# Kernel tuning notes

Hardware: AMD Instinct MI355X
Metric: run time of the kernel (lower is better)

## Reference

```python
import jax, jax.numpy as jnp
import numpy as np

N_ENT, N_REL, N_TIME, N_METAREL = 20000, 400, 366, 800
E, PE = 200000, 80000
ENT, REL, TIME = 160, 160, 80
NUM_LAYERS = 2
NL = 2 * NUM_LAYERS + 2  # enc layers + dec layers + mean + log_std
DIN_E = REL + ENT + TIME
DIN_R = 2 * REL


def setup_inputs() -> dict:
    key = jax.random.key(0)
    ks = jax.random.split(key, 40)
    s = 0.05
    inp = {
        "ent_feat": jax.random.normal(ks[0], (N_ENT, ENT), jnp.float32),
        "rel_feat": jax.random.normal(ks[1], (N_REL, REL), jnp.float32),
        "time_emb": jax.random.normal(ks[2], (N_TIME, TIME), jnp.float32),
        "metarel_emb": jax.random.normal(ks[3], (N_METAREL, REL), jnp.float32),
        "noise_e": jax.random.normal(ks[4], (N_ENT, ENT), jnp.float32),
        "noise_r": jax.random.normal(ks[5], (N_REL, REL), jnp.float32),
        "ent_WI_w": jax.random.normal(ks[6], (NL, DIN_E, ENT), jnp.float32) * s,
        "ent_WI_b": jnp.zeros((NL, ENT), jnp.float32),
        "ent_WO_w": jax.random.normal(ks[7], (NL, DIN_E, ENT), jnp.float32) * s,
        "ent_WO_b": jnp.zeros((NL, ENT), jnp.float32),
        "ent_WS_w": jax.random.normal(ks[8], (NL, ENT, ENT), jnp.float32) * s,
        "ent_WS_b": jnp.zeros((NL, ENT), jnp.float32),
        "ent_WT_w": jax.random.normal(ks[9], (NL, TIME, TIME), jnp.float32) * s,
        "ent_WT_b": jnp.zeros((NL, TIME), jnp.float32),
        "rel_WI_w": jax.random.normal(ks[10], (NL, DIN_R, REL), jnp.float32) * s,
        "rel_WI_b": jnp.zeros((NL, REL), jnp.float32),
        "rel_WO_w": jax.random.normal(ks[11], (NL, DIN_R, REL), jnp.float32) * s,
        "rel_WO_b": jnp.zeros((NL, REL), jnp.float32),
        "rel_WS_w": jax.random.normal(ks[12], (NL, REL, REL), jnp.float32) * s,
        "rel_WS_b": jnp.zeros((NL, REL), jnp.float32),
        "rel_WM_w": jax.random.normal(ks[13], (NL, REL, REL), jnp.float32) * s,
        "rel_WM_b": jnp.zeros((NL, REL), jnp.float32),
        "src": jax.random.randint(ks[14], (E,), 0, N_ENT, jnp.int32),
        "dst": jax.random.randint(ks[15], (E,), 0, N_ENT, jnp.int32),
        "e_rel": jax.random.randint(ks[16], (E,), 0, N_REL, jnp.int32),
        "e_time": jax.random.randint(ks[17], (E,), 0, N_TIME, jnp.int32),
        "e_inv": jax.random.randint(ks[18], (E,), 0, 2, jnp.int32),
        "p_src": jax.random.randint(ks[19], (PE,), 0, N_REL, jnp.int32),
        "p_dst": jax.random.randint(ks[20], (PE,), 0, N_REL, jnp.int32),
        "p_rel": jax.random.randint(ks[21], (PE,), 0, N_METAREL, jnp.int32),
        "p_inv": jax.random.randint(ks[22], (PE,), 0, 2, jnp.int32),
    }
    return inp


def _mean_agg(msg, dst, n_nodes):
    # DGL fn.mean: zero for nodes with no in-edges
    s = jax.ops.segment_sum(msg, dst, num_segments=n_nodes)
    c = jax.ops.segment_sum(jnp.ones((msg.shape[0], 1), msg.dtype), dst, num_segments=n_nodes)
    return jnp.where(c > 0, s / jnp.maximum(c, 1.0), jnp.zeros_like(s))


def _ent_layer(p, i, ent, rel, tim, src, dst, e_rel, e_time, e_inv, act):
    (WIw, WIb, WOw, WOb, WSw, WSb, WTw, WTb) = p
    comp = jnp.concatenate([rel[e_rel], ent[src], tim[e_time]], axis=-1)  # [E, rel+ent+time]
    msg = jnp.where((e_inv == 0)[:, None], comp @ WIw[i] + WIb[i], comp @ WOw[i] + WOb[i])
    h_agg = _mean_agg(msg, dst, ent.shape[0])
    h = ent @ WSw[i] + WSb[i] + h_agg
    t = tim @ WTw[i] + WTb[i]
    if act:
        h, t = jax.nn.relu(h), jax.nn.relu(t)
    return h, t


def _rel_layer(p, i, rel, meta, p_src, p_dst, p_rel, p_inv, act):
    (WIw, WIb, WOw, WOb, WSw, WSb, WMw, WMb) = p
    comp = jnp.concatenate([meta[p_rel], rel[p_src]], axis=-1)  # [PE, 2*rel]
    msg = jnp.where((p_inv == 0)[:, None], comp @ WIw[i] + WIb[i], comp @ WOw[i] + WOb[i])
    h_agg = _mean_agg(msg, p_dst, rel.shape[0])
    h = rel @ WSw[i] + WSb[i] + h_agg
    m = meta @ WMw[i] + WMb[i]
    if act:
        h, m = jax.nn.relu(h), jax.nn.relu(m)
    return h, m


def _vgae(ent, rel, tim, meta, noise_e, noise_r, pe, pr, g, pg):
    L = NUM_LAYERS
    # encoder GNN: layers 0..L-1
    for i in range(L):
        act = i < L - 1
        ent, tim = _ent_layer(pe, i, ent, rel, tim, *g, act)
        rel, meta = _rel_layer(pr, i, rel, meta, *pg, act)
    # variational heads: indices 2L (mean), 2L+1 (log_std), act=None
    mean_e = _ent_layer(pe, 2 * L, ent, rel, tim, *g, False)[0]
    log_std_e = _ent_layer(pe, 2 * L + 1, ent, rel, tim, *g, False)[0]
    mean_r = _rel_layer(pr, 2 * L, rel, meta, *pg, False)[0]
    log_std_r = _rel_layer(pr, 2 * L + 1, rel, meta, *pg, False)[0]
    z_e = mean_e + noise_e * jnp.exp(log_std_e)
    z_r = mean_r + noise_r * jnp.exp(log_std_r)
    # decoder GNN: layers L..2L-1, starting from sampled z
    ent_o, rel_o, tim_o, meta_o = z_e, z_r, tim, meta
    for i in range(L):
        act = i < L - 1
        ent_o, tim_o = _ent_layer(pe, L + i, ent_o, rel_o, tim_o, *g, act)
        rel_o, meta_o = _rel_layer(pr, L + i, rel_o, meta_o, *pg, act)
    return (ent, ent_o, rel, rel_o, tim, tim_o, meta, meta_o)


def reference(ent_feat, rel_feat, time_emb, metarel_emb, noise_e, noise_r,
              ent_WI_w, ent_WI_b, ent_WO_w, ent_WO_b, ent_WS_w, ent_WS_b, ent_WT_w, ent_WT_b,
              rel_WI_w, rel_WI_b, rel_WO_w, rel_WO_b, rel_WS_w, rel_WS_b, rel_WM_w, rel_WM_b,
              src, dst, e_rel, e_time, e_inv, p_src, p_dst, p_rel, p_inv):
    pe = (ent_WI_w, ent_WI_b, ent_WO_w, ent_WO_b, ent_WS_w, ent_WS_b, ent_WT_w, ent_WT_b)
    pr = (rel_WI_w, rel_WI_b, rel_WO_w, rel_WO_b, rel_WS_w, rel_WS_b, rel_WM_w, rel_WM_b)
    g = (src, dst, e_rel, e_time, e_inv)
    pg = (p_src, p_dst, p_rel, p_inv)
    return _vgae(ent_feat, rel_feat, time_emb, metarel_emb, noise_e, noise_r, pe, pr, g, pg)
```

## Files before the change

kernel.cpp:

```cpp
#include <hip/hip_runtime.h>
#include <math.h>

#define N_ENT     20000
#define N_RELN    400
#define N_TIME    366
#define N_META    800
#define NE        200000
#define NPE       80000

typedef __attribute__((ext_vector_type(8))) short short8;
typedef __attribute__((ext_vector_type(4))) float f32x4;

static __device__ __forceinline__ ushort f2bf(float x) {
    unsigned u = __float_as_uint(x);
    unsigned r = (u + 0x7FFF + ((u >> 16) & 1)) >> 16;
    return (ushort)r;
}
static __device__ __forceinline__ float bf2f(ushort b) {
    return __uint_as_float(((unsigned)b) << 16);
}

struct BPrep { const float* W[18]; };

__global__ __launch_bounds__(256) void bprep(BPrep bp, ushort* __restrict__ hi, ushort* __restrict__ lo)
{
    int idx = blockIdx.x * 256 + threadIdx.x;
    if (idx >= 18 * 160 * 20) return;
    int s = idx / 3200, rem = idx - s * 3200;
    int n = rem / 20, kc = rem - n * 20;
    const float* __restrict__ W = bp.W[s];
    ushort h[8], l[8];
#pragma unroll
    for (int j = 0; j < 8; ++j) {
        float x = W[(kc * 8 + j) * 160 + n];
        h[j] = f2bf(x);
        l[j] = f2bf(x - bf2f(h[j]));
    }
    size_t o = (size_t)s * 25600 + n * 160 + kc * 8;
    *(short8*)(hi + o) = *(short8*)h;
    *(short8*)(lo + o) = *(short8*)l;
}

__global__ __launch_bounds__(256) void aprep(const float* __restrict__ in,
                                             ushort* __restrict__ hi, ushort* __restrict__ lo, int n8)
{
    int i = blockIdx.x * 256 + threadIdx.x;
    if (i >= n8) return;
    const float* p = in + (size_t)i * 8;
    ushort h[8], l[8];
#pragma unroll
    for (int j = 0; j < 8; ++j) {
        float x = p[j];
        h[j] = f2bf(x);
        l[j] = f2bf(x - bf2f(h[j]));
    }
    *(short8*)(hi + (size_t)i * 8) = *(short8*)h;
    *(short8*)(lo + (size_t)i * 8) = *(short8*)l;
}

struct BigMF {
    const ushort* bh[3];
    const ushort* bl[3];
    const float*  bias[3];
    float*        C[3];
};

__global__ __launch_bounds__(256, 4) void gemm_big_mfma(
    const ushort* __restrict__ Ah, const ushort* __restrict__ Al, int M, BigMF bb)
{
    __shared__ ushort Ahi[64][40], Alo[64][40];
    __shared__ ushort Bhi[160][40], Blo[160][40];
    const int z = blockIdx.z;
    const ushort* __restrict__ Bh = bb.bh[z];
    const ushort* __restrict__ Bl = bb.bl[z];
    const float*  __restrict__ bias = bb.bias[z];
    float* __restrict__ C = bb.C[z];
    const int m0 = blockIdx.x * 64;
    const int t  = threadIdx.x;
    const int lane = t & 63, w = t >> 6;
    const int fr = lane & 15, fq = lane >> 4;

    f32x4 acc[10];
#pragma unroll
    for (int i = 0; i < 10; ++i) acc[i] = (f32x4){0.f, 0.f, 0.f, 0.f};

    for (int k0 = 0; k0 < 160; k0 += 32) {
        {
            int r = t >> 2, kc = t & 3;
            int row = m0 + r;
            short8 vh = {0,0,0,0,0,0,0,0}, vl = {0,0,0,0,0,0,0,0};
            if (row < M) {
                size_t o = (size_t)row * 160 + k0 + kc * 8;
                vh = *(const short8*)(Ah + o);
                vl = *(const short8*)(Al + o);
            }
            *(short8*)&Ahi[r][kc * 8] = vh;
            *(short8*)&Alo[r][kc * 8] = vl;
        }
#pragma unroll
        for (int i = 0; i < 3; ++i) {
            int idx = t + i * 256;
            if (idx < 640) {
                int col = idx >> 2, kc = idx & 3;
                size_t o = (size_t)col * 160 + k0 + kc * 8;
                *(short8*)&Bhi[col][kc * 8] = *(const short8*)(Bh + o);
                *(short8*)&Blo[col][kc * 8] = *(const short8*)(Bl + o);
            }
        }
        __syncthreads();
        short8 ah = *(const short8*)&Ahi[w * 16 + fr][fq * 8];
        short8 al = *(const short8*)&Alo[w * 16 + fr][fq * 8];
#pragma unroll
        for (int tt = 0; tt < 10; ++tt) {
            short8 bh = *(const short8*)&Bhi[tt * 16 + fr][fq * 8];
            short8 bl = *(const short8*)&Blo[tt * 16 + fr][fq * 8];
            acc[tt] = __builtin_amdgcn_mfma_f32_16x16x32_bf16(ah, bh, acc[tt], 0, 0, 0);
            acc[tt] = __builtin_amdgcn_mfma_f32_16x16x32_bf16(al, bh, acc[tt], 0, 0, 0);
            acc[tt] = __builtin_amdgcn_mfma_f32_16x16x32_bf16(ah, bl, acc[tt], 0, 0, 0);
        }
        __syncthreads();
    }
#pragma unroll
    for (int tt = 0; tt < 10; ++tt) {
        int col = tt * 16 + fr;
        float bv = bias ? bias[col] : 0.f;
#pragma unroll
        for (int q = 0; q < 4; ++q) {
            int row = m0 + w * 16 + fq * 4 + q;
            if (row < M) C[(size_t)row * 160 + col] = acc[tt][q] + bv;
        }
    }
}

struct SmallDesc {
    const float* A;
    const float* B;
    const float* bias;
    float*       C;
    int M, K, N, ldb, relu;
};
struct SmallBatch { SmallDesc d[18]; };

#define FMA4(acc, a, b) { acc.x = fmaf(a, b.x, acc.x); acc.y = fmaf(a, b.y, acc.y); \
                          acc.z = fmaf(a, b.z, acc.z); acc.w = fmaf(a, b.w, acc.w); }

__global__ __launch_bounds__(256) void gemm_small_batch(SmallBatch sb)
{
    SmallDesc dd = sb.d[blockIdx.y];
    int tid = blockIdx.x * 256 + threadIdx.x;
    int ng = dd.N >> 2;
    int mb = tid / ng;
    int nmb = (dd.M + 3) >> 2;
    if (mb >= nmb) return;
    int g = tid - mb * ng;
    int r0 = mb * 4;
    int mlast = dd.M - 1;
    const float* A0 = dd.A + (size_t)min(r0 + 0, mlast) * dd.K;
    const float* A1 = dd.A + (size_t)min(r0 + 1, mlast) * dd.K;
    const float* A2 = dd.A + (size_t)min(r0 + 2, mlast) * dd.K;
    const float* A3 = dd.A + (size_t)min(r0 + 3, mlast) * dd.K;
    const float* Bp = dd.B + g * 4;
    float4 c0 = {0,0,0,0}, c1 = {0,0,0,0}, c2 = {0,0,0,0}, c3 = {0,0,0,0};
    for (int k = 0; k < dd.K; k += 4) {
        float4 b0 = *(const float4*)(Bp + (size_t)(k + 0) * dd.ldb);
        float4 b1 = *(const float4*)(Bp + (size_t)(k + 1) * dd.ldb);
        float4 b2 = *(const float4*)(Bp + (size_t)(k + 2) * dd.ldb);
        float4 b3 = *(const float4*)(Bp + (size_t)(k + 3) * dd.ldb);
        float4 a0 = *(const float4*)(A0 + k);
        float4 a1 = *(const float4*)(A1 + k);
        float4 a2 = *(const float4*)(A2 + k);
        float4 a3 = *(const float4*)(A3 + k);
        FMA4(c0, a0.x, b0) FMA4(c0, a0.y, b1) FMA4(c0, a0.z, b2) FMA4(c0, a0.w, b3)
        FMA4(c1, a1.x, b0) FMA4(c1, a1.y, b1) FMA4(c1, a1.z, b2) FMA4(c1, a1.w, b3)
        FMA4(c2, a2.x, b0) FMA4(c2, a2.y, b1) FMA4(c2, a2.z, b2) FMA4(c2, a2.w, b3)
        FMA4(c3, a3.x, b0) FMA4(c3, a3.y, b1) FMA4(c3, a3.z, b2) FMA4(c3, a3.w, b3)
    }
    float4 bv = {0,0,0,0};
    if (dd.bias) bv = *(const float4*)(dd.bias + g * 4);
    c0.x += bv.x; c0.y += bv.y; c0.z += bv.z; c0.w += bv.w;
    c1.x += bv.x; c1.y += bv.y; c1.z += bv.z; c1.w += bv.w;
    c2.x += bv.x; c2.y += bv.y; c2.z += bv.z; c2.w += bv.w;
    c3.x += bv.x; c3.y += bv.y; c3.z += bv.z; c3.w += bv.w;
    if (dd.relu) {
        c0.x = fmaxf(c0.x, 0.f); c0.y = fmaxf(c0.y, 0.f); c0.z = fmaxf(c0.z, 0.f); c0.w = fmaxf(c0.w, 0.f);
        c1.x = fmaxf(c1.x, 0.f); c1.y = fmaxf(c1.y, 0.f); c1.z = fmaxf(c1.z, 0.f); c1.w = fmaxf(c1.w, 0.f);
        c2.x = fmaxf(c2.x, 0.f); c2.y = fmaxf(c2.y, 0.f); c2.z = fmaxf(c2.z, 0.f); c2.w = fmaxf(c2.w, 0.f);
        c3.x = fmaxf(c3.x, 0.f); c3.y = fmaxf(c3.y, 0.f); c3.z = fmaxf(c3.z, 0.f); c3.w = fmaxf(c3.w, 0.f);
    }
    float* C = dd.C + (size_t)r0 * dd.N + g * 4;
    if (r0 + 0 < dd.M) *(float4*)(C + 0 * (size_t)dd.N) = c0;
    if (r0 + 1 < dd.M) *(float4*)(C + 1 * (size_t)dd.N) = c1;
    if (r0 + 2 < dd.M) *(float4*)(C + 2 * (size_t)dd.N) = c2;
    if (r0 + 3 < dd.M) *(float4*)(C + 3 * (size_t)dd.N) = c3;
}

__global__ void count_deg(const int* __restrict__ d, int E, int* __restrict__ cnt)
{
    int e = blockIdx.x * 256 + threadIdx.x;
    if (e < E) atomicAdd(&cnt[d[e]], 1);
}

__global__ __launch_bounds__(256) void scan_excl(int* __restrict__ cnt, int* __restrict__ rowptr, int n)
{
    __shared__ int ssum[256];
    int t = threadIdx.x;
    int chunk = (n + 255) / 256;
    int s0 = t * chunk; if (s0 > n) s0 = n;
    int s1 = s0 + chunk; if (s1 > n) s1 = n;
    int local = 0;
    for (int i = s0; i < s1; ++i) local += cnt[i];
    ssum[t] = local;
    __syncthreads();
    if (t == 0) {
        int acc = 0;
        for (int i = 0; i < 256; ++i) { int v = ssum[i]; ssum[i] = acc; acc += v; }
        rowptr[n] = acc;
    }
    __syncthreads();
    int acc = ssum[t];
    for (int i = s0; i < s1; ++i) {
        int v = cnt[i];
        rowptr[i] = acc;
        cnt[i] = acc;
        acc += v;
    }
}

__global__ void scatter_pack(const int* __restrict__ d, const int* __restrict__ a0,
                             const int* __restrict__ a1, const int* __restrict__ a2,
                             const int* __restrict__ inv, int E,
                             int* __restrict__ cursor, int4* __restrict__ pack)
{
    int e = blockIdx.x * 256 + threadIdx.x;
    if (e < E) {
        int p = atomicAdd(&cursor[d[e]], 1);
        int4 v;
        v.x = a0[e]; v.y = a1[e]; v.z = a2 ? a2[e] : 0; v.w = inv[e];
        pack[p] = v;
    }
}

__global__ __launch_bounds__(256) void agg_ent_csr(
    const int* __restrict__ rowptr, const int4* __restrict__ pack,
    const float* __restrict__ arI, const float* __restrict__ arO,
    const float* __restrict__ aeI, const float* __restrict__ aeO,
    const float* __restrict__ atI, const float* __restrict__ atO,
    float* __restrict__ H, int relu)
{
    int tid = blockIdx.x * 256 + threadIdx.x;
    int n = tid / 40;
    if (n >= N_ENT) return;
    int g = tid - n * 40;
    int c = g * 4;
    int b = rowptr[n], e = rowptr[n + 1];
    float ax = 0.f, ay = 0.f, az = 0.f, aw = 0.f;
    for (int j = b; j < e; ++j) {
        int4 p = pack[j];
        const float* t1 = (p.w ? arO : arI) + (size_t)p.x * 160 + c;
        const float* t2 = (p.w ? aeO : aeI) + (size_t)p.y * 160 + c;
        const float* t3 = (p.w ? atO : atI) + (size_t)p.z * 160 + c;
        float4 v1 = *(const float4*)t1;
        float4 v2 = *(const float4*)t2;
        float4 v3 = *(const float4*)t3;
        ax += v1.x + v2.x + v3.x;
        ay += v1.y + v2.y + v3.y;
        az += v1.z + v2.z + v3.z;
        aw += v1.w + v2.w + v3.w;
    }
    size_t idx = (size_t)n * 160 + c;
    float4 h = *(const float4*)(H + idx);
    if (e > b) {
        float s = 1.0f / (float)(e - b);
        h.x = fmaf(ax, s, h.x); h.y = fmaf(ay, s, h.y);
        h.z = fmaf(az, s, h.z); h.w = fmaf(aw, s, h.w);
    }
    if (relu) {
        h.x = fmaxf(h.x, 0.f); h.y = fmaxf(h.y, 0.f);
        h.z = fmaxf(h.z, 0.f); h.w = fmaxf(h.w, 0.f);
    }
    *(float4*)(H + idx) = h;
}

__global__ __launch_bounds__(256) void agg_ent_sample(
    const int* __restrict__ rowptr, const int4* __restrict__ pack,
    const float* __restrict__ arI, const float* __restrict__ arO,
    const float* __restrict__ aeI, const float* __restrict__ aeO,
    const float* __restrict__ atI, const float* __restrict__ atO,
    const float* __restrict__ Hs, const float* __restrict__ mean,
    const float* __restrict__ noise, float* __restrict__ out)
{
    int tid = blockIdx.x * 256 + threadIdx.x;
    int n = tid / 40;
    if (n >= N_ENT) return;
    int g = tid - n * 40;
    int c = g * 4;
    int b = rowptr[n], e = rowptr[n + 1];
    float ax = 0.f, ay = 0.f, az = 0.f, aw = 0.f;
    for (int j = b; j < e; ++j) {
        int4 p = pack[j];
        const float* t1 = (p.w ? arO : arI) + (size_t)p.x * 160 + c;
        const float* t2 = (p.w ? aeO : aeI) + (size_t)p.y * 160 + c;
        const float* t3 = (p.w ? atO : atI) + (size_t)p.z * 160 + c;
        float4 v1 = *(const float4*)t1;
        float4 v2 = *(const float4*)t2;
        float4 v3 = *(const float4*)t3;
        ax += v1.x + v2.x + v3.x;
        ay += v1.y + v2.y + v3.y;
        az += v1.z + v2.z + v3.z;
        aw += v1.w + v2.w + v3.w;
    }
    size_t idx = (size_t)n * 160 + c;
    float4 h = *(const float4*)(Hs + idx);
    if (e > b) {
        float s = 1.0f / (float)(e - b);
        h.x = fmaf(ax, s, h.x); h.y = fmaf(ay, s, h.y);
        h.z = fmaf(az, s, h.z); h.w = fmaf(aw, s, h.w);
    }
    float4 mn = *(const float4*)(mean + idx);
    float4 nz = *(const float4*)(noise + idx);
    float4 zv;
    zv.x = fmaf(nz.x, expf(h.x), mn.x);
    zv.y = fmaf(nz.y, expf(h.y), mn.y);
    zv.z = fmaf(nz.z, expf(h.z), mn.z);
    zv.w = fmaf(nz.w, expf(h.w), mn.w);
    *(float4*)(out + idx) = zv;
}

__global__ __launch_bounds__(512) void agg_rel_fused(
    const int* __restrict__ rowptr, const int4* __restrict__ pack,
    const float* __restrict__ bmI, const float* __restrict__ bmO,
    const float* __restrict__ brI, const float* __restrict__ brO,
    float* __restrict__ H, int relu)
{
    __shared__ float part[12][40][4];
    int n = blockIdx.x;
    int t = threadIdx.x;
    int g = t % 40, s = t / 40;
    int b = rowptr[n], e = rowptr[n + 1];
    if (s < 12) {
        int c = g * 4;
        float ax = 0.f, ay = 0.f, az = 0.f, aw = 0.f;
        for (int j = b + s; j < e; j += 12) {
            int4 p = pack[j];
            const float* pm = (p.w ? bmO : bmI) + (size_t)p.x * 160 + c;
            const float* pr = (p.w ? brO : brI) + (size_t)p.y * 160 + c;
            float4 vm = *(const float4*)pm;
            float4 vr = *(const float4*)pr;
            ax += vm.x + vr.x; ay += vm.y + vr.y;
            az += vm.z + vr.z; aw += vm.w + vr.w;
        }
        part[s][g][0] = ax; part[s][g][1] = ay;
        part[s][g][2] = az; part[s][g][3] = aw;
    }
    __syncthreads();
    if (t < 160) {
        int gg = t >> 2, q = t & 3;
        float acc = 0.f;
#pragma unroll
        for (int s2 = 0; s2 < 12; ++s2) acc += part[s2][gg][q];
        size_t idx = (size_t)n * 160 + t;
        float h = H[idx];
        int d = e - b;
        if (d > 0) h = fmaf(acc, 1.0f / (float)d, h);
        if (relu) h = fmaxf(h, 0.f);
        H[idx] = h;
    }
}

__global__ __launch_bounds__(512) void agg_rel_sample(
    const int* __restrict__ rowptr, const int4* __restrict__ pack,
    const float* __restrict__ bmI, const float* __restrict__ bmO,
    const float* __restrict__ brI, const float* __restrict__ brO,
    const float* __restrict__ Hs, const float* __restrict__ mean,
    const float* __restrict__ noise, float* __restrict__ out)
{
    __shared__ float part[12][40][4];
    int n = blockIdx.x;
    int t = threadIdx.x;
    int g = t % 40, s = t / 40;
    int b = rowptr[n], e = rowptr[n + 1];
    if (s < 12) {
        int c = g * 4;
        float ax = 0.f, ay = 0.f, az = 0.f, aw = 0.f;
        for (int j = b + s; j < e; j += 12) {
            int4 p = pack[j];
            const float* pm = (p.w ? bmO : bmI) + (size_t)p.x * 160 + c;
            const float* pr = (p.w ? brO : brI) + (size_t)p.y * 160 + c;
            float4 vm = *(const float4*)pm;
            float4 vr = *(const float4*)pr;
            ax += vm.x + vr.x; ay += vm.y + vr.y;
            az += vm.z + vr.z; aw += vm.w + vr.w;
        }
        part[s][g][0] = ax; part[s][g][1] = ay;
        part[s][g][2] = az; part[s][g][3] = aw;
    }
    __syncthreads();
    if (t < 160) {
        int gg = t >> 2, q = t & 3;
        float acc = 0.f;
#pragma unroll
        for (int s2 = 0; s2 < 12; ++s2) acc += part[s2][gg][q];
        size_t idx = (size_t)n * 160 + t;
        float h = Hs[idx];
        int d = e - b;
        if (d > 0) h = fmaf(acc, 1.0f / (float)d, h);
        out[idx] = fmaf(noise[idx], expf(h), mean[idx]);
    }
}

extern "C" void kernel_launch(void* const* d_in, const int* in_sizes, int n_in,
                              void* d_out, int out_size, void* d_ws, size_t ws_size,
                              hipStream_t stream)
{
    const float* ent0   = (const float*)d_in[0];
    const float* rel0   = (const float*)d_in[1];
    const float* tim0   = (const float*)d_in[2];
    const float* meta0  = (const float*)d_in[3];
    const float* noiseE = (const float*)d_in[4];
    const float* noiseR = (const float*)d_in[5];
    const float* entWI  = (const float*)d_in[6];
    const float* entWIb = (const float*)d_in[7];
    const float* entWO  = (const float*)d_in[8];
    const float* entWOb = (const float*)d_in[9];
    const float* entWS  = (const float*)d_in[10];
    const float* entWSb = (const float*)d_in[11];
    const float* entWT  = (const float*)d_in[12];
    const float* entWTb = (const float*)d_in[13];
    const float* relWI  = (const float*)d_in[14];
    const float* relWIb = (const float*)d_in[15];
    const float* relWO  = (const float*)d_in[16];
    const float* relWOb = (const float*)d_in[17];
    const float* relWS  = (const float*)d_in[18];
    const float* relWSb = (const float*)d_in[19];
    const float* relWM  = (const float*)d_in[20];
    const float* relWMb = (const float*)d_in[21];
    const int* src    = (const int*)d_in[22];
    const int* dst    = (const int*)d_in[23];
    const int* e_rel  = (const int*)d_in[24];
    const int* e_time = (const int*)d_in[25];
    const int* e_inv  = (const int*)d_in[26];
    const int* p_src  = (const int*)d_in[27];
    const int* p_dst  = (const int*)d_in[28];
    const int* p_rel  = (const int*)d_in[29];
    const int* p_inv  = (const int*)d_in[30];

    float* out = (float*)d_out;
    float* OUT_ent   = out + 0;
    float* OUT_ento  = out + 3200000;
    float* OUT_rel   = out + 6400000;
    float* OUT_relo  = out + 6464000;
    float* OUT_tim   = out + 6528000;
    float* OUT_timo  = out + 6557280;
    float* OUT_meta  = out + 6586560;
    float* OUT_metao = out + 6714560;

    char* wsp = (char*)d_ws;
    size_t off = 0;
    auto allocF = [&](size_t n) -> float* {
        float* p = (float*)(wsp + off);
        off += ((n * sizeof(float) + 255) & ~(size_t)255);
        return p;
    };
    auto allocU = [&](size_t n) -> ushort* {
        ushort* p = (ushort*)(wsp + off);
        off += ((n * sizeof(ushort) + 255) & ~(size_t)255);
        return p;
    };
    auto allocI = [&](size_t n) -> int* {
        int* p = (int*)(wsp + off);
        off += ((n * sizeof(int) + 255) & ~(size_t)255);
        return p;
    };
    float* AI      = allocF(3200000);
    float* AO      = allocF(3200000);
    float* B1v     = allocF(3200000);
    float* B5v     = allocF(3200000);
    float* tim1    = allocF(29280);
    float* tim_o1  = allocF(29280);
    float* rel1    = allocF(64000);
    float* rel_o1  = allocF(64000);
    float* meta1   = allocF(128000);
    float* meta_o1 = allocF(128000);
    float* arI  = allocF(64000);
    float* arO  = allocF(64000);
    float* atI  = allocF(58560);
    float* atO  = allocF(58560);
    float* bmI  = allocF(128000);
    float* bmO  = allocF(128000);
    float* brI  = allocF(64000);
    float* brO  = allocF(64000);
    float* ar5I = allocF(64000);
    float* ar5O = allocF(64000);
    float* at5I = allocF(58560);
    float* at5O = allocF(58560);
    float* bm5I = allocF(128000);
    float* bm5O = allocF(128000);
    float* br5I = allocF(64000);
    float* br5O = allocF(64000);
    float* hR4  = allocF(64000);
    float* hR5  = allocF(64000);
    float* zR   = allocF(64000);
    ushort* Ahg = allocU(3200000);
    ushort* Alg = allocU(3200000);
    ushort* Bhg = allocU(18 * 25600);
    ushort* Blg = allocU(18 * 25600);
    int*  cntE    = allocI(N_ENT);
    int*  rowptrE = allocI(N_ENT + 1);
    int4* packE   = (int4*)allocI(NE * 4);
    int*  cntR    = allocI(N_RELN);
    int*  rowptrR = allocI(N_RELN + 1);
    int4* packR   = (int4*)allocI(NPE * 4);
    if (ws_size < off) return;

    hipMemsetAsync(cntE, 0, N_ENT * sizeof(int), stream);
    hipMemsetAsync(cntR, 0, N_RELN * sizeof(int), stream);
    count_deg<<<(NE + 255) / 256, 256, 0, stream>>>(dst, NE, cntE);
    count_deg<<<(NPE + 255) / 256, 256, 0, stream>>>(p_dst, NPE, cntR);
    scan_excl<<<1, 256, 0, stream>>>(cntE, rowptrE, N_ENT);
    scan_excl<<<1, 256, 0, stream>>>(cntR, rowptrR, N_RELN);
    scatter_pack<<<(NE + 255) / 256, 256, 0, stream>>>(dst, e_rel, src, e_time, e_inv, NE, cntE, packE);
    scatter_pack<<<(NPE + 255) / 256, 256, 0, stream>>>(p_dst, p_rel, p_src, nullptr, p_inv, NPE, cntR, packR);

    BPrep bp;
    for (int li = 0; li < 6; ++li) {
        bp.W[li * 3 + 0] = entWI + (size_t)li * 64000 + 25600;
        bp.W[li * 3 + 1] = entWO + (size_t)li * 64000 + 25600;
        bp.W[li * 3 + 2] = entWS + (size_t)li * 25600;
    }
    bprep<<<(18 * 160 * 20 + 255) / 256, 256, 0, stream>>>(bp, Bhg, Blg);

    auto big3 = [&](int li, float* entOut) {
        BigMF bb;
        for (int j = 0; j < 3; ++j) {
            bb.bh[j] = Bhg + (size_t)(li * 3 + j) * 25600;
            bb.bl[j] = Blg + (size_t)(li * 3 + j) * 25600;
        }
        bb.bias[0] = nullptr; bb.bias[1] = nullptr; bb.bias[2] = entWSb + li * 160;
        bb.C[0] = AI; bb.C[1] = AO; bb.C[2] = entOut;
        gemm_big_mfma<<<dim3(313, 1, 3), 256, 0, stream>>>(Ahg, Alg, N_ENT, bb);
    };
    auto prepA = [&](const float* entIn) {
        aprep<<<(400000 + 255) / 256, 256, 0, stream>>>(entIn, Ahg, Alg, 400000);
    };

    auto stage = [&](int li, const float* entIn, const float* relIn, const float* timIn,
                     const float* metaIn, float* entOut, float* timOut,
                     float* relOut, float* metaOut, int act) {
        const float* WI  = entWI + (size_t)li * 64000;
        const float* WO  = entWO + (size_t)li * 64000;
        const float* rWI = relWI + (size_t)li * 51200;
        const float* rWO = relWO + (size_t)li * 51200;

        SmallBatch sb{};
        int ns = 0;
        sb.d[ns++] = SmallDesc{relIn,  WI,          entWIb + li * 160, arI,    N_RELN, 160, 160, 160, 0};
        sb.d[ns++] = SmallDesc{relIn,  WO,          entWOb + li * 160, arO,    N_RELN, 160, 160, 160, 0};
        sb.d[ns++] = SmallDesc{timIn,  WI + 51200,  nullptr,           atI,    N_TIME,  80, 160, 160, 0};
        sb.d[ns++] = SmallDesc{timIn,  WO + 51200,  nullptr,           atO,    N_TIME,  80, 160, 160, 0};
        if (timOut)
            sb.d[ns++] = SmallDesc{timIn, entWT + (size_t)li * 6400, entWTb + li * 80,
                                   timOut, N_TIME, 80, 80, 80, act};
        sb.d[ns++] = SmallDesc{metaIn, rWI,         relWIb + li * 160, bmI,    N_META, 160, 160, 160, 0};
        sb.d[ns++] = SmallDesc{metaIn, rWO,         relWOb + li * 160, bmO,    N_META, 160, 160, 160, 0};
        sb.d[ns++] = SmallDesc{relIn,  rWI + 25600, nullptr,           brI,    N_RELN, 160, 160, 160, 0};
        sb.d[ns++] = SmallDesc{relIn,  rWO + 25600, nullptr,           brO,    N_RELN, 160, 160, 160, 0};
        sb.d[ns++] = SmallDesc{relIn,  relWS + (size_t)li * 25600, relWSb + li * 160,
                               relOut, N_RELN, 160, 160, 160, 0};
        if (metaOut)
            sb.d[ns++] = SmallDesc{metaIn, relWM + (size_t)li * 25600, relWMb + li * 160,
                                   metaOut, N_META, 160, 160, 160, act};
        gemm_small_batch<<<dim3(32, ns), 256, 0, stream>>>(sb);

        prepA(entIn);
        big3(li, entOut);
        agg_ent_csr<<<(N_ENT * 40 + 255) / 256, 256, 0, stream>>>(
            rowptrE, packE, arI, arO, AI, AO, atI, atO, entOut, act);
        agg_rel_fused<<<N_RELN, 512, 0, stream>>>(
            rowptrR, packR, bmI, bmO, brI, brO, relOut, act);
    };

    stage(0, ent0, rel0, tim0, meta0, B1v, tim1, rel1, meta1, 1);
    stage(1, B1v, rel1, tim1, meta1, OUT_ent, OUT_tim, OUT_rel, OUT_meta, 0);

    {
        const float* WI4  = entWI + (size_t)4 * 64000;
        const float* WO4  = entWO + (size_t)4 * 64000;
        const float* WI5  = entWI + (size_t)5 * 64000;
        const float* WO5  = entWO + (size_t)5 * 64000;
        const float* rWI4 = relWI + (size_t)4 * 51200;
        const float* rWO4 = relWO + (size_t)4 * 51200;
        const float* rWI5 = relWI + (size_t)5 * 51200;
        const float* rWO5 = relWO + (size_t)5 * 51200;

        SmallBatch sb{};
        int ns = 0;
        sb.d[ns++] = SmallDesc{OUT_rel,  WI4,          entWIb + 4 * 160, arI,  N_RELN, 160, 160, 160, 0};
        sb.d[ns++] = SmallDesc{OUT_rel,  WO4,          entWOb + 4 * 160, arO,  N_RELN, 160, 160, 160, 0};
        sb.d[ns++] = SmallDesc{OUT_tim,  WI4 + 51200,  nullptr,          atI,  N_TIME,  80, 160, 160, 0};
        sb.d[ns++] = SmallDesc{OUT_tim,  WO4 + 51200,  nullptr,          atO,  N_TIME,  80, 160, 160, 0};
        sb.d[ns++] = SmallDesc{OUT_meta, rWI4,         relWIb + 4 * 160, bmI,  N_META, 160, 160, 160, 0};
        sb.d[ns++] = SmallDesc{OUT_meta, rWO4,         relWOb + 4 * 160, bmO,  N_META, 160, 160, 160, 0};
        sb.d[ns++] = SmallDesc{OUT_rel,  rWI4 + 25600, nullptr,          brI,  N_RELN, 160, 160, 160, 0};
        sb.d[ns++] = SmallDesc{OUT_rel,  rWO4 + 25600, nullptr,          brO,  N_RELN, 160, 160, 160, 0};
        sb.d[ns++] = SmallDesc{OUT_rel,  relWS + (size_t)4 * 25600, relWSb + 4 * 160,
                               hR4, N_RELN, 160, 160, 160, 0};
        sb.d[ns++] = SmallDesc{OUT_rel,  WI5,          entWIb + 5 * 160, ar5I, N_RELN, 160, 160, 160, 0};
        sb.d[ns++] = SmallDesc{OUT_rel,  WO5,          entWOb + 5 * 160, ar5O, N_RELN, 160, 160, 160, 0};
        sb.d[ns++] = SmallDesc{OUT_tim,  WI5 + 51200,  nullptr,          at5I, N_TIME,  80, 160, 160, 0};
        sb.d[ns++] = SmallDesc{OUT_tim,  WO5 + 51200,  nullptr,          at5O, N_TIME,  80, 160, 160, 0};
        sb.d[ns++] = SmallDesc{OUT_meta, rWI5,         relWIb + 5 * 160, bm5I, N_META, 160, 160, 160, 0};
        sb.d[ns++] = SmallDesc{OUT_meta, rWO5,         relWOb + 5 * 160, bm5O, N_META, 160, 160, 160, 0};
        sb.d[ns++] = SmallDesc{OUT_rel,  rWI5 + 25600, nullptr,          br5I, N_RELN, 160, 160, 160, 0};
        sb.d[ns++] = SmallDesc{OUT_rel,  rWO5 + 25600, nullptr,          br5O, N_RELN, 160, 160, 160, 0};
        sb.d[ns++] = SmallDesc{OUT_rel,  relWS + (size_t)5 * 25600, relWSb + 5 * 160,
                               hR5, N_RELN, 160, 160, 160, 0};
        gemm_small_batch<<<dim3(32, ns), 256, 0, stream>>>(sb);

        prepA(OUT_ent);
        big3(4, B5v);
        agg_ent_csr<<<(N_ENT * 40 + 255) / 256, 256, 0, stream>>>(
            rowptrE, packE, arI, arO, AI, AO, atI, atO, B5v, 0);
        big3(5, B1v);
        agg_ent_sample<<<(N_ENT * 40 + 255) / 256, 256, 0, stream>>>(
            rowptrE, packE, ar5I, ar5O, AI, AO, at5I, at5O, B1v, B5v, noiseE, B5v);
        agg_rel_fused<<<N_RELN, 512, 0, stream>>>(
            rowptrR, packR, bmI, bmO, brI, brO, hR4, 0);
        agg_rel_sample<<<N_RELN, 512, 0, stream>>>(
            rowptrR, packR, bm5I, bm5O, br5I, br5O, hR5, hR4, noiseR, zR);
    }

    stage(2, B5v, zR, OUT_tim, OUT_meta, B1v, tim_o1, rel_o1, meta_o1, 1);
    stage(3, B1v, rel_o1, tim_o1, meta_o1, OUT_ento, OUT_timo, OUT_relo, OUT_metao, 0);
}
```

Baseline: 857.9 us.

## Merge independent kernels into role-dispatched launches to cut launch count

Independent work is packed into shared launches selected by blockIdx.y. The small GEMM batch now runs alongside the A-matrix bf16 split, the relation aggregation shares a launch with the big MFMA GEMM, and the entity and relation sampling heads are combined into one kernel. Graph preprocessing is also merged: one degree count, one 1024-thread warp-shuffle scan and one scatter handle both graphs. This removes launches and serialization gaps and lets the small relation work overlap the large GEMM, but the relation aggregation now uses 6 partial sums instead of 12, giving it less per-node parallelism.

```diff
diff --git a/kernel.cpp b/kernel.cpp
--- a/kernel.cpp
+++ b/kernel.cpp
@@ -39,97 +39,6 @@
     size_t o = (size_t)s * 25600 + n * 160 + kc * 8;
     *(short8*)(hi + o) = *(short8*)h;
     *(short8*)(lo + o) = *(short8*)l;
-}
-
-__global__ __launch_bounds__(256) void aprep(const float* __restrict__ in,
-                                             ushort* __restrict__ hi, ushort* __restrict__ lo, int n8)
-{
-    int i = blockIdx.x * 256 + threadIdx.x;
-    if (i >= n8) return;
-    const float* p = in + (size_t)i * 8;
-    ushort h[8], l[8];
-#pragma unroll
-    for (int j = 0; j < 8; ++j) {
-        float x = p[j];
-        h[j] = f2bf(x);
-        l[j] = f2bf(x - bf2f(h[j]));
-    }
-    *(short8*)(hi + (size_t)i * 8) = *(short8*)h;
-    *(short8*)(lo + (size_t)i * 8) = *(short8*)l;
-}
-
-struct BigMF {
-    const ushort* bh[3];
-    const ushort* bl[3];
-    const float*  bias[3];
-    float*        C[3];
-};
-
-__global__ __launch_bounds__(256, 4) void gemm_big_mfma(
-    const ushort* __restrict__ Ah, const ushort* __restrict__ Al, int M, BigMF bb)
-{
-    __shared__ ushort Ahi[64][40], Alo[64][40];
-    __shared__ ushort Bhi[160][40], Blo[160][40];
-    const int z = blockIdx.z;
-    const ushort* __restrict__ Bh = bb.bh[z];
-    const ushort* __restrict__ Bl = bb.bl[z];
-    const float*  __restrict__ bias = bb.bias[z];
-    float* __restrict__ C = bb.C[z];
-    const int m0 = blockIdx.x * 64;
-    const int t  = threadIdx.x;
-    const int lane = t & 63, w = t >> 6;
-    const int fr = lane & 15, fq = lane >> 4;
-
-    f32x4 acc[10];
-#pragma unroll
-    for (int i = 0; i < 10; ++i) acc[i] = (f32x4){0.f, 0.f, 0.f, 0.f};
-
-    for (int k0 = 0; k0 < 160; k0 += 32) {
-        {
-            int r = t >> 2, kc = t & 3;
-            int row = m0 + r;
-            short8 vh = {0,0,0,0,0,0,0,0}, vl = {0,0,0,0,0,0,0,0};
-            if (row < M) {
-                size_t o = (size_t)row * 160 + k0 + kc * 8;
-                vh = *(const short8*)(Ah + o);
-                vl = *(const short8*)(Al + o);
-            }
-            *(short8*)&Ahi[r][kc * 8] = vh;
-            *(short8*)&Alo[r][kc * 8] = vl;
-        }
-#pragma unroll
-        for (int i = 0; i < 3; ++i) {
-            int idx = t + i * 256;
-            if (idx < 640) {
-                int col = idx >> 2, kc = idx & 3;
-                size_t o = (size_t)col * 160 + k0 + kc * 8;
-                *(short8*)&Bhi[col][kc * 8] = *(const short8*)(Bh + o);
-                *(short8*)&Blo[col][kc * 8] = *(const short8*)(Bl + o);
-            }
-        }
-        __syncthreads();
-        short8 ah = *(const short8*)&Ahi[w * 16 + fr][fq * 8];
-        short8 al = *(const short8*)&Alo[w * 16 + fr][fq * 8];
-#pragma unroll
-        for (int tt = 0; tt < 10; ++tt) {
-            short8 bh = *(const short8*)&Bhi[tt * 16 + fr][fq * 8];
-            short8 bl = *(const short8*)&Blo[tt * 16 + fr][fq * 8];
-            acc[tt] = __builtin_amdgcn_mfma_f32_16x16x32_bf16(ah, bh, acc[tt], 0, 0, 0);
-            acc[tt] = __builtin_amdgcn_mfma_f32_16x16x32_bf16(al, bh, acc[tt], 0, 0, 0);
-            acc[tt] = __builtin_amdgcn_mfma_f32_16x16x32_bf16(ah, bl, acc[tt], 0, 0, 0);
-        }
-        __syncthreads();
-    }
-#pragma unroll
-    for (int tt = 0; tt < 10; ++tt) {
-        int col = tt * 16 + fr;
-        float bv = bias ? bias[col] : 0.f;
-#pragma unroll
-        for (int q = 0; q < 4; ++q) {
-            int row = m0 + w * 16 + fq * 4 + q;
-            if (row < M) C[(size_t)row * 160 + col] = acc[tt][q] + bv;
-        }
-    }
 }
 
 struct SmallDesc {
@@ -144,10 +53,28 @@
 #define FMA4(acc, a, b) { acc.x = fmaf(a, b.x, acc.x); acc.y = fmaf(a, b.y, acc.y); \
                           acc.z = fmaf(a, b.z, acc.z); acc.w = fmaf(a, b.w, acc.w); }
 
-__global__ __launch_bounds__(256) void gemm_small_batch(SmallBatch sb)
-{
-    SmallDesc dd = sb.d[blockIdx.y];
+__global__ __launch_bounds__(256) void stage_p1(SmallBatch sb, int ns,
+    const float* __restrict__ ain, ushort* __restrict__ ah, ushort* __restrict__ al, int nitems)
+{
+    int role = blockIdx.y;
     int tid = blockIdx.x * 256 + threadIdx.x;
+    if (role == ns) {
+        int stride = gridDim.x * 256;
+        for (int i = tid; i < nitems; i += stride) {
+            const float* p = ain + (size_t)i * 8;
+            ushort h[8], l[8];
+#pragma unroll
+            for (int j = 0; j < 8; ++j) {
+                float x = p[j];
+                h[j] = f2bf(x);
+                l[j] = f2bf(x - bf2f(h[j]));
+            }
+            *(short8*)(ah + (size_t)i * 8) = *(short8*)h;
+            *(short8*)(al + (size_t)i * 8) = *(short8*)l;
+        }
+        return;
+    }
+    SmallDesc dd = sb.d[role];
     int ng = dd.N >> 2;
     int mb = tid / ng;
     int nmb = (dd.M + 3) >> 2;
@@ -194,49 +121,124 @@
     if (r0 + 3 < dd.M) *(float4*)(C + 3 * (size_t)dd.N) = c3;
 }
 
-__global__ void count_deg(const int* __restrict__ d, int E, int* __restrict__ cnt)
-{
-    int e = blockIdx.x * 256 + threadIdx.x;
-    if (e < E) atomicAdd(&cnt[d[e]], 1);
-}
-
-__global__ __launch_bounds__(256) void scan_excl(int* __restrict__ cnt, int* __restrict__ rowptr, int n)
-{
-    __shared__ int ssum[256];
-    int t = threadIdx.x;
-    int chunk = (n + 255) / 256;
-    int s0 = t * chunk; if (s0 > n) s0 = n;
-    int s1 = s0 + chunk; if (s1 > n) s1 = n;
-    int local = 0;
-    for (int i = s0; i < s1; ++i) local += cnt[i];
-    ssum[t] = local;
+struct BigMF {
+    const ushort* bh[3];
+    const ushort* bl[3];
+    const float*  bias[3];
+    float*        C[3];
+};
+struct AggRelA {
+    const int* rowptr;
+    const int4* pack;
+    const float *bmI, *bmO, *brI, *brO;
+    float* H;
+    int relu;
+};
+
+__global__ __launch_bounds__(256, 4) void stage_p2(
+    const ushort* __restrict__ Ah, const ushort* __restrict__ Al, int M,
+    BigMF bb, AggRelA ar)
+{
+    __shared__ ushort Ahi[64][40], Alo[64][40];
+    __shared__ ushort Bhi[160][40], Blo[160][40];
+    __shared__ float part[6][40][4];
+    const int role = blockIdx.y;
+    const int t = threadIdx.x;
+
+    if (role < 3) {
+        const int m0 = blockIdx.x * 64;
+        if (m0 >= M) return;
+        const ushort* __restrict__ Bh = bb.bh[role];
+        const ushort* __restrict__ Bl = bb.bl[role];
+        const float*  __restrict__ bias = bb.bias[role];
+        float* __restrict__ C = bb.C[role];
+        const int lane = t & 63, w = t >> 6;
+        const int fr = lane & 15, fq = lane >> 4;
+
+        f32x4 acc[10];
+#pragma unroll
+        for (int i = 0; i < 10; ++i) acc[i] = (f32x4){0.f, 0.f, 0.f, 0.f};
+
+        for (int k0 = 0; k0 < 160; k0 += 32) {
+            {
+                int r = t >> 2, kc = t & 3;
+                int row = m0 + r;
+                short8 vh = {0,0,0,0,0,0,0,0}, vl = {0,0,0,0,0,0,0,0};
+                if (row < M) {
+                    size_t o = (size_t)row * 160 + k0 + kc * 8;
+                    vh = *(const short8*)(Ah + o);
+                    vl = *(const short8*)(Al + o);
+                }
+                *(short8*)&Ahi[r][kc * 8] = vh;
+                *(short8*)&Alo[r][kc * 8] = vl;
+            }
+#pragma unroll
+            for (int i = 0; i < 3; ++i) {
+                int idx = t + i * 256;
+                if (idx < 640) {
+                    int col = idx >> 2, kc = idx & 3;
+                    size_t o = (size_t)col * 160 + k0 + kc * 8;
+                    *(short8*)&Bhi[col][kc * 8] = *(const short8*)(Bh + o);
+                    *(short8*)&Blo[col][kc * 8] = *(const short8*)(Bl + o);
+                }
+            }
+            __syncthreads();
+            short8 ahv = *(const short8*)&Ahi[w * 16 + fr][fq * 8];
+            short8 alv = *(const short8*)&Alo[w * 16 + fr][fq * 8];
+#pragma unroll
+            for (int tt = 0; tt < 10; ++tt) {
+                short8 bh = *(const short8*)&Bhi[tt * 16 + fr][fq * 8];
+                short8 bl = *(const short8*)&Blo[tt * 16 + fr][fq * 8];
+                acc[tt] = __builtin_amdgcn_mfma_f32_16x16x32_bf16(ahv, bh, acc[tt], 0, 0, 0);
+                acc[tt] = __builtin_amdgcn_mfma_f32_16x16x32_bf16(alv, bh, acc[tt], 0, 0, 0);
+                acc[tt] = __builtin_amdgcn_mfma_f32_16x16x32_bf16(ahv, bl, acc[tt], 0, 0, 0);
+            }
+            __syncthreads();
+        }
+#pragma unroll
+        for (int tt = 0; tt < 10; ++tt) {
+            int col = tt * 16 + fr;
+            float bv = bias ? bias[col] : 0.f;
+#pragma unroll
+            for (int q = 0; q < 4; ++q) {
+                int row = m0 + w * 16 + fq * 4 + q;
+                if (row < M) C[(size_t)row * 160 + col] = acc[tt][q] + bv;
+            }
+        }
+        return;
+    }
+
+    int n = blockIdx.x;
+    if (n >= N_RELN) return;
+    int g = t % 40, s = t / 40;
+    int b = ar.rowptr[n], e = ar.rowptr[n + 1];
+    if (s < 6) {
+        int c = g * 4;
+        float ax = 0.f, ay = 0.f, az = 0.f, aw = 0.f;
+        for (int j = b + s; j < e; j += 6) {
+            int4 p = ar.pack[j];
+            const float* pm = (p.w ? ar.bmO : ar.bmI) + (size_t)p.x * 160 + c;
+            const float* pr = (p.w ? ar.brO : ar.brI) + (size_t)p.y * 160 + c;
+            float4 vm = *(const float4*)pm;
+            float4 vr = *(const float4*)pr;
+            ax += vm.x + vr.x; ay += vm.y + vr.y;
+            az += vm.z + vr.z; aw += vm.w + vr.w;
+        }
+        part[s][g][0] = ax; part[s][g][1] = ay;
+        part[s][g][2] = az; part[s][g][3] = aw;
+    }
     __syncthreads();
-    if (t == 0) {
-        int acc = 0;
-        for (int i = 0; i < 256; ++i) { int v = ssum[i]; ssum[i] = acc; acc += v; }
-        rowptr[n] = acc;
-    }
-    __syncthreads();
-    int acc = ssum[t];
-    for (int i = s0; i < s1; ++i) {
-        int v = cnt[i];
-        rowptr[i] = acc;
-        cnt[i] = acc;
-        acc += v;
-    }
-}
-
-__global__ void scatter_pack(const int* __restrict__ d, const int* __restrict__ a0,
-                             const int* __restrict__ a1, const int* __restrict__ a2,
-                             const int* __restrict__ inv, int E,
-                             int* __restrict__ cursor, int4* __restrict__ pack)
-{
-    int e = blockIdx.x * 256 + threadIdx.x;
-    if (e < E) {
-        int p = atomicAdd(&cursor[d[e]], 1);
-        int4 v;
-        v.x = a0[e]; v.y = a1[e]; v.z = a2 ? a2[e] : 0; v.w = inv[e];
-        pack[p] = v;
+    if (t < 160) {
+        int gg = t >> 2, q = t & 3;
+        float acc = 0.f;
+#pragma unroll
+        for (int s2 = 0; s2 < 6; ++s2) acc += part[s2][gg][q];
+        size_t idx = (size_t)n * 160 + t;
+        float h = ar.H[idx];
+        int d = e - b;
+        if (d > 0) h = fmaf(acc, 1.0f / (float)d, h);
+        if (ar.relu) h = fmaxf(h, 0.f);
+        ar.H[idx] = h;
     }
 }
 
@@ -281,67 +283,68 @@
     *(float4*)(H + idx) = h;
 }
 
-__global__ __launch_bounds__(256) void agg_ent_sample(
-    const int* __restrict__ rowptr, const int4* __restrict__ pack,
+__global__ __launch_bounds__(256) void heads_p3b(
+    const int* __restrict__ rowptrE, const int4* __restrict__ packE,
     const float* __restrict__ arI, const float* __restrict__ arO,
     const float* __restrict__ aeI, const float* __restrict__ aeO,
     const float* __restrict__ atI, const float* __restrict__ atO,
-    const float* __restrict__ Hs, const float* __restrict__ mean,
-    const float* __restrict__ noise, float* __restrict__ out)
-{
-    int tid = blockIdx.x * 256 + threadIdx.x;
-    int n = tid / 40;
-    if (n >= N_ENT) return;
-    int g = tid - n * 40;
-    int c = g * 4;
-    int b = rowptr[n], e = rowptr[n + 1];
-    float ax = 0.f, ay = 0.f, az = 0.f, aw = 0.f;
-    for (int j = b; j < e; ++j) {
-        int4 p = pack[j];
-        const float* t1 = (p.w ? arO : arI) + (size_t)p.x * 160 + c;
-        const float* t2 = (p.w ? aeO : aeI) + (size_t)p.y * 160 + c;
-        const float* t3 = (p.w ? atO : atI) + (size_t)p.z * 160 + c;
-        float4 v1 = *(const float4*)t1;
-        float4 v2 = *(const float4*)t2;
-        float4 v3 = *(const float4*)t3;
-        ax += v1.x + v2.x + v3.x;
-        ay += v1.y + v2.y + v3.y;
-        az += v1.z + v2.z + v3.z;
-        aw += v1.w + v2.w + v3.w;
-    }
-    size_t idx = (size_t)n * 160 + c;
-    float4 h = *(const float4*)(Hs + idx);
-    if (e > b) {
-        float s = 1.0f / (float)(e - b);
-        h.x = fmaf(ax, s, h.x); h.y = fmaf(ay, s, h.y);
-        h.z = fmaf(az, s, h.z); h.w = fmaf(aw, s, h.w);
-    }
-    float4 mn = *(const float4*)(mean + idx);
-    float4 nz = *(const float4*)(noise + idx);
-    float4 zv;
-    zv.x = fmaf(nz.x, expf(h.x), mn.x);
-    zv.y = fmaf(nz.y, expf(h.y), mn.y);
-    zv.z = fmaf(nz.z, expf(h.z), mn.z);
-    zv.w = fmaf(nz.w, expf(h.w), mn.w);
-    *(float4*)(out + idx) = zv;
-}
-
-__global__ __launch_bounds__(512) void agg_rel_fused(
-    const int* __restrict__ rowptr, const int4* __restrict__ pack,
+    const float* __restrict__ HsE, const float* __restrict__ meanE,
+    const float* __restrict__ noiseE, float* __restrict__ outE,
+    const int* __restrict__ rowptrR, const int4* __restrict__ packR,
     const float* __restrict__ bmI, const float* __restrict__ bmO,
     const float* __restrict__ brI, const float* __restrict__ brO,
-    float* __restrict__ H, int relu)
-{
-    __shared__ float part[12][40][4];
+    const float* __restrict__ HsR, const float* __restrict__ meanR,
+    const float* __restrict__ noiseR, float* __restrict__ outR)
+{
+    __shared__ float part[6][40][4];
+    const int t = threadIdx.x;
+    if (blockIdx.y == 0) {
+        int tid = blockIdx.x * 256 + t;
+        int n = tid / 40;
+        if (n >= N_ENT) return;
+        int g = tid - n * 40;
+        int c = g * 4;
+        int b = rowptrE[n], e = rowptrE[n + 1];
+        float ax = 0.f, ay = 0.f, az = 0.f, aw = 0.f;
+        for (int j = b; j < e; ++j) {
+            int4 p = packE[j];
+            const float* t1 = (p.w ? arO : arI) + (size_t)p.x * 160 + c;
+            const float* t2 = (p.w ? aeO : aeI) + (size_t)p.y * 160 + c;
+            const float* t3 = (p.w ? atO : atI) + (size_t)p.z * 160 + c;
+            float4 v1 = *(const float4*)t1;
+            float4 v2 = *(const float4*)t2;
+            float4 v3 = *(const float4*)t3;
+            ax += v1.x + v2.x + v3.x;
+            ay += v1.y + v2.y + v3.y;
+            az += v1.z + v2.z + v3.z;
+            aw += v1.w + v2.w + v3.w;
+        }
+        size_t idx = (size_t)n * 160 + c;
+        float4 h = *(const float4*)(HsE + idx);
+        if (e > b) {
+            float s = 1.0f / (float)(e - b);
+            h.x = fmaf(ax, s, h.x); h.y = fmaf(ay, s, h.y);
+            h.z = fmaf(az, s, h.z); h.w = fmaf(aw, s, h.w);
+        }
+        float4 mn = *(const float4*)(meanE + idx);
+        float4 nz = *(const float4*)(noiseE + idx);
+        float4 zv;
+        zv.x = fmaf(nz.x, expf(h.x), mn.x);
+        zv.y = fmaf(nz.y, expf(h.y), mn.y);
+        zv.z = fmaf(nz.z, expf(h.z), mn.z);
+        zv.w = fmaf(nz.w, expf(h.w), mn.w);
+        *(float4*)(outE + idx) = zv;
+        return;
+    }
     int n = blockIdx.x;
-    int t = threadIdx.x;
+    if (n >= N_RELN) return;
     int g = t % 40, s = t / 40;
-    int b = rowptr[n], e = rowptr[n + 1];
-    if (s < 12) {
+    int b = rowptrR[n], e = rowptrR[n + 1];
+    if (s < 6) {
         int c = g * 4;
         float ax = 0.f, ay = 0.f, az = 0.f, aw = 0.f;
-        for (int j = b + s; j < e; j += 12) {
-            int4 p = pack[j];
+        for (int j = b + s; j < e; j += 6) {
+            int4 p = packR[j];
             const float* pm = (p.w ? bmO : bmI) + (size_t)p.x * 160 + c;
             const float* pr = (p.w ? brO : brI) + (size_t)p.y * 160 + c;
             float4 vm = *(const float4*)pm;
@@ -357,54 +360,84 @@
         int gg = t >> 2, q = t & 3;
         float acc = 0.f;
 #pragma unroll
-        for (int s2 = 0; s2 < 12; ++s2) acc += part[s2][gg][q];
+        for (int s2 = 0; s2 < 6; ++s2) acc += part[s2][gg][q];
         size_t idx = (size_t)n * 160 + t;
-        float h = H[idx];
+        float h = HsR[idx];
         int d = e - b;
         if (d > 0) h = fmaf(acc, 1.0f / (float)d, h);
-        if (relu) h = fmaxf(h, 0.f);
-        H[idx] = h;
-    }
-}
-
-__global__ __launch_bounds__(512) void agg_rel_sample(
-    const int* __restrict__ rowptr, const int4* __restrict__ pack,
-    const float* __restrict__ bmI, const float* __restrict__ bmO,
-    const float* __restrict__ brI, const float* __restrict__ brO,
-    const float* __restrict__ Hs, const float* __restrict__ mean,
-    const float* __restrict__ noise, float* __restrict__ out)
-{
-    __shared__ float part[12][40][4];
-    int n = blockIdx.x;
-    int t = threadIdx.x;
-    int g = t % 40, s = t / 40;
-    int b = rowptr[n], e = rowptr[n + 1];
-    if (s < 12) {
-        int c = g * 4;
-        float ax = 0.f, ay = 0.f, az = 0.f, aw = 0.f;
-        for (int j = b + s; j < e; j += 12) {
-            int4 p = pack[j];
-            const float* pm = (p.w ? bmO : bmI) + (size_t)p.x * 160 + c;
-            const float* pr = (p.w ? brO : brI) + (size_t)p.y * 160 + c;
-            float4 vm = *(const float4*)pm;
-            float4 vr = *(const float4*)pr;
-            ax += vm.x + vr.x; ay += vm.y + vr.y;
-            az += vm.z + vr.z; aw += vm.w + vr.w;
-        }
-        part[s][g][0] = ax; part[s][g][1] = ay;
-        part[s][g][2] = az; part[s][g][3] = aw;
-    }
+        outR[idx] = fmaf(noiseR[idx], expf(h), meanR[idx]);
+    }
+}
+
+__global__ void count2(const int* __restrict__ d1, int E1, int* __restrict__ c1,
+                       const int* __restrict__ d2, int E2, int* __restrict__ c2)
+{
+    int e = blockIdx.x * 256 + threadIdx.x;
+    if (blockIdx.y == 0) { if (e < E1) atomicAdd(&c1[d1[e]], 1); }
+    else                 { if (e < E2) atomicAdd(&c2[d2[e]], 1); }
+}
+
+static __device__ void scan_body(int* __restrict__ cnt, int* __restrict__ rowptr,
+                                 int n, int* __restrict__ wsum)
+{
+    int t = threadIdx.x, lane = t & 63, w = t >> 6;
+    int chunk = (n + 1023) >> 10;
+    int s0 = t * chunk; if (s0 > n) s0 = n;
+    int s1 = s0 + chunk; if (s1 > n) s1 = n;
+    int local = 0;
+    for (int i = s0; i < s1; ++i) local += cnt[i];
+    int incl = local;
+#pragma unroll
+    for (int d = 1; d < 64; d <<= 1) {
+        int v = __shfl_up(incl, d, 64);
+        if (lane >= d) incl += v;
+    }
+    if (lane == 63) wsum[w] = incl;
     __syncthreads();
-    if (t < 160) {
-        int gg = t >> 2, q = t & 3;
-        float acc = 0.f;
-#pragma unroll
-        for (int s2 = 0; s2 < 12; ++s2) acc += part[s2][gg][q];
-        size_t idx = (size_t)n * 160 + t;
-        float h = Hs[idx];
-        int d = e - b;
-        if (d > 0) h = fmaf(acc, 1.0f / (float)d, h);
-        out[idx] = fmaf(noise[idx], expf(h), mean[idx]);
+    if (t == 0) {
+        int a = 0;
+#pragma unroll
+        for (int i = 0; i < 16; ++i) { int v = wsum[i]; wsum[i] = a; a += v; }
+    }
+    __syncthreads();
+    int acc = wsum[w] + incl - local;
+    for (int i = s0; i < s1; ++i) {
+        int v = cnt[i];
+        rowptr[i] = acc;
+        cnt[i] = acc;
+        acc += v;
+    }
+    if (t == 1023) rowptr[n] = acc;
+}
+
+__global__ __launch_bounds__(1024) void scan2(int* cntE, int* rowptrE, int* cntR, int* rowptrR)
+{
+    __shared__ int wsum[16];
+    if (blockIdx.x == 0) scan_body(cntE, rowptrE, N_ENT, wsum);
+    else                 scan_body(cntR, rowptrR, N_RELN, wsum);
+}
+
+__global__ void scatter2(
+    const int* __restrict__ d1, const int* __restrict__ a10, const int* __restrict__ a11,
+    const int* __restrict__ a12, const int* __restrict__ inv1, int E1,
+    int* __restrict__ cur1, int4* __restrict__ pk1,
+    const int* __restrict__ d2, const int* __restrict__ a20, const int* __restrict__ a21,
+    const int* __restrict__ inv2, int E2,
+    int* __restrict__ cur2, int4* __restrict__ pk2)
+{
+    int e = blockIdx.x * 256 + threadIdx.x;
+    if (blockIdx.y == 0) {
+        if (e < E1) {
+            int p = atomicAdd(&cur1[d1[e]], 1);
+            int4 v; v.x = a10[e]; v.y = a11[e]; v.z = a12[e]; v.w = inv1[e];
+            pk1[p] = v;
+        }
+    } else {
+        if (e < E2) {
+            int p = atomicAdd(&cur2[d2[e]], 1);
+            int4 v; v.x = a20[e]; v.y = a21[e]; v.z = 0; v.w = inv2[e];
+            pk2[p] = v;
+        }
     }
 }
 
@@ -514,12 +547,10 @@
 
     hipMemsetAsync(cntE, 0, N_ENT * sizeof(int), stream);
     hipMemsetAsync(cntR, 0, N_RELN * sizeof(int), stream);
-    count_deg<<<(NE + 255) / 256, 256, 0, stream>>>(dst, NE, cntE);
-    count_deg<<<(NPE + 255) / 256, 256, 0, stream>>>(p_dst, NPE, cntR);
-    scan_excl<<<1, 256, 0, stream>>>(cntE, rowptrE, N_ENT);
-    scan_excl<<<1, 256, 0, stream>>>(cntR, rowptrR, N_RELN);
-    scatter_pack<<<(NE + 255) / 256, 256, 0, stream>>>(dst, e_rel, src, e_time, e_inv, NE, cntE, packE);
-    scatter_pack<<<(NPE + 255) / 256, 256, 0, stream>>>(p_dst, p_rel, p_src, nullptr, p_inv, NPE, cntR, packR);
+    count2<<<dim3(782, 2), 256, 0, stream>>>(dst, NE, cntE, p_dst, NPE, cntR);
+    scan2<<<2, 1024, 0, stream>>>(cntE, rowptrE, cntR, rowptrR);
+    scatter2<<<dim3(782, 2), 256, 0, stream>>>(dst, e_rel, src, e_time, e_inv, NE, cntE, packE,
+                                               p_dst, p_rel, p_src, p_inv, NPE, cntR, packR);
 
     BPrep bp;
     for (int li = 0; li < 6; ++li) {
@@ -529,7 +560,7 @@
     }
     bprep<<<(18 * 160 * 20 + 255) / 256, 256, 0, stream>>>(bp, Bhg, Blg);
 
-    auto big3 = [&](int li, float* entOut) {
+    auto bigmf = [&](int li, float* entOut) -> BigMF {
         BigMF bb;
         for (int j = 0; j < 3; ++j) {
             bb.bh[j] = Bhg + (size_t)(li * 3 + j) * 25600;
@@ -537,10 +568,7 @@
         }
         bb.bias[0] = nullptr; bb.bias[1] = nullptr; bb.bias[2] = entWSb + li * 160;
         bb.C[0] = AI; bb.C[1] = AO; bb.C[2] = entOut;
-        gemm_big_mfma<<<dim3(313, 1, 3), 256, 0, stream>>>(Ahg, Alg, N_ENT, bb);
-    };
-    auto prepA = [&](const float* entIn) {
-        aprep<<<(400000 + 255) / 256, 256, 0, stream>>>(entIn, Ahg, Alg, 400000);
+        return bb;
     };
 
     auto stage = [&](int li, const float* entIn, const float* relIn, const float* timIn,
@@ -569,14 +597,13 @@
         if (metaOut)
             sb.d[ns++] = SmallDesc{metaIn, relWM + (size_t)li * 25600, relWMb + li * 160,
                                    metaOut, N_META, 160, 160, 160, act};
-        gemm_small_batch<<<dim3(32, ns), 256, 0, stream>>>(sb);
-
-        prepA(entIn);
-        big3(li, entOut);
-        agg_ent_csr<<<(N_ENT * 40 + 255) / 256, 256, 0, stream>>>(
+        stage_p1<<<dim3(128, ns + 1), 256, 0, stream>>>(sb, ns, entIn, Ahg, Alg, 400000);
+
+        AggRelA ar{rowptrR, packR, bmI, bmO, brI, brO, relOut, act};
+        stage_p2<<<dim3(400, 4), 256, 0, stream>>>(Ahg, Alg, N_ENT, bigmf(li, entOut), ar);
+
+        agg_ent_csr<<<3125, 256, 0, stream>>>(
             rowptrE, packE, arI, arO, AI, AO, atI, atO, entOut, act);
-        agg_rel_fused<<<N_RELN, 512, 0, stream>>>(
-            rowptrR, packR, bmI, bmO, brI, brO, relOut, act);
     };
 
     stage(0, ent0, rel0, tim0, meta0, B1v, tim1, rel1, meta1, 1);
@@ -614,18 +641,16 @@
         sb.d[ns++] = SmallDesc{OUT_rel,  rWO5 + 25600, nullptr,          br5O, N_RELN, 160, 160, 160, 0};
         sb.d[ns++] = SmallDesc{OUT_rel,  relWS + (size_t)5 * 25600, relWSb + 5 * 160,
                                hR5, N_RELN, 160, 160, 160, 0};
-        gemm_small_batch<<<dim3(32, ns), 256, 0, stream>>>(sb);
-
-        prepA(OUT_ent);
-        big3(4, B5v);
-        agg_ent_csr<<<(N_ENT * 40 + 255) / 256, 256, 0, stream>>>(
+        stage_p1<<<dim3(128, ns + 1), 256, 0, stream>>>(sb, ns, OUT_ent, Ahg, Alg, 400000);
+
+        AggRelA ar4{rowptrR, packR, bmI, bmO, brI, brO, hR4, 0};
+        stage_p2<<<dim3(400, 4), 256, 0, stream>>>(Ahg, Alg, N_ENT, bigmf(4, B5v), ar4);
+        agg_ent_csr<<<3125, 256, 0, stream>>>(
             rowptrE, packE, arI, arO, AI, AO, atI, atO, B5v, 0);
-        big3(5, B1v);
-        agg_ent_sample<<<(N_ENT * 40 + 255) / 256, 256, 0, stream>>>(
-            rowptrE, packE, ar5I, ar5O, AI, AO, at5I, at5O, B1v, B5v, noiseE, B5v);
-        agg_rel_fused<<<N_RELN, 512, 0, stream>>>(
-            rowptrR, packR, bmI, bmO, brI, brO, hR4, 0);
-        agg_rel_sample<<<N_RELN, 512, 0, stream>>>(
+        AggRelA arNull{};
+        stage_p2<<<dim3(313, 3), 256, 0, stream>>>(Ahg, Alg, N_ENT, bigmf(5, B1v), arNull);
+        heads_p3b<<<dim3(3125, 2), 256, 0, stream>>>(
+            rowptrE, packE, ar5I, ar5O, AI, AO, at5I, at5O, B1v, B5v, noiseE, B5v,
             rowptrR, packR, bm5I, bm5O, br5I, br5O, hR5, hR4, noiseR, zR);
     }
 
```

Result: slower. 936.9 us (+9.2%).
